# Performance work log

Measured on AMD Instinct MI355X. Metric: run time of the kernel, lower is better.

Reference implementation:

```python
import jax, jax.numpy as jnp
import numpy as np
from functools import partial

IMG_H, IMG_W = 800.0, 800.0
PRE_NMS_TOP_N = 6000
POST_NMS_TOP_N = 1000
MIN_BOX_SIZE = 16.0
NMS_THRESH = 0.7
B, N = 4, 100000


def setup_inputs() -> dict:
    key = jax.random.key(0)
    k1, k2, k3 = jax.random.split(key, 3)
    # plausible boxes: centers in image, sizes in [1, 201] so some fail the min-size test
    ctr = jax.random.uniform(k1, (B, N, 2), dtype=jnp.float32) * jnp.array([IMG_W, IMG_H], jnp.float32)
    wh = jax.random.uniform(k2, (B, N, 2), dtype=jnp.float32) * 200.0 + 1.0
    batch_proposals = jnp.concatenate([ctr - wh / 2.0, ctr + wh / 2.0], axis=-1)  # [B,N,4] x1,y1,x2,y2
    batch_cls_prob = jax.random.uniform(k3, (B, N, 2), dtype=jnp.float32)  # [B,N,2] bg/fg
    return {"batch_proposals": batch_proposals, "batch_cls_prob": batch_cls_prob}


def _clip_boxes(boxes):
    # matches torch clamp of x coords to [0,W], y coords to [0,H]
    x = jnp.clip(boxes[:, 0::2], 0.0, IMG_W)  # [N,2] -> x1,x2
    y = jnp.clip(boxes[:, 1::2], 0.0, IMG_H)  # [N,2] -> y1,y2
    return jnp.stack([x, y], axis=2).reshape(boxes.shape)  # interleave back to x1,y1,x2,y2


def _iou_matrix(b):
    x1, y1, x2, y2 = b[:, 0], b[:, 1], b[:, 2], b[:, 3]
    area = jnp.maximum(x2 - x1, 0.0) * jnp.maximum(y2 - y1, 0.0)  # [P]
    xx1 = jnp.maximum(x1[:, None], x1[None, :])
    yy1 = jnp.maximum(y1[:, None], y1[None, :])
    xx2 = jnp.minimum(x2[:, None], x2[None, :])
    yy2 = jnp.minimum(y2[:, None], y2[None, :])
    inter = jnp.maximum(xx2 - xx1, 0.0) * jnp.maximum(yy2 - yy1, 0.0)  # [P,P]
    union = area[:, None] + area[None, :] - inter
    return inter / jnp.maximum(union, 1e-9)


def _greedy_nms_keep(iou, valid):
    # boxes are already sorted by score (descending); standard greedy suppression
    P = iou.shape[0]
    idx = jnp.arange(P)

    def body(i, keep):
        sup = keep[i] & (iou[i] > NMS_THRESH) & (idx > i)
        return keep & ~sup

    return jax.lax.fori_loop(0, P, body, valid)


def _per_image(boxes, scores):
    boxes = _clip_boxes(boxes)  # [N,4]
    w = boxes[:, 2] - boxes[:, 0]
    h = boxes[:, 3] - boxes[:, 1]
    valid = (w >= MIN_BOX_SIZE) & (h >= MIN_BOX_SIZE)
    # filter-then-topk == mask invalid to -inf then topk (assuming >= PRE valid boxes)
    s_masked = jnp.where(valid, scores, -jnp.inf)
    top_s, top_idx = jax.lax.top_k(s_masked, PRE_NMS_TOP_N)
    b = boxes[top_idx]            # [P,4]
    v = valid[top_idx]            # [P]
    keep = _greedy_nms_keep(_iou_matrix(b), v)
    s2 = jnp.where(keep, top_s, -jnp.inf)
    fin_s, fin_idx = jax.lax.top_k(s2, POST_NMS_TOP_N)  # kept boxes, score order
    fin_keep = keep[fin_idx]
    fin_b = jnp.where(fin_keep[:, None], b[fin_idx], 0.0)
    fin_s = jnp.where(fin_keep, fin_s, 0.0)  # zero-pad if fewer than POST kept
    return fin_s, fin_b


def reference(batch_proposals, batch_cls_prob):
    scores = batch_cls_prob[:, :, 1]  # fg prob
    final_scores, final_boxes = jax.vmap(_per_image)(batch_proposals, scores)
    return final_scores, final_boxes  # [B,POST], [B,POST,4]
```

## Files before the change

kernel.cpp:

```cpp
#include <hip/hip_runtime.h>
#include <hip/hip_bf16.h>
#include <math.h>

typedef unsigned int uint;
typedef unsigned short ushort;
typedef unsigned long long u64;

#define BB 4
#define NN 100000
#define PRE 6000
#define POST 1000
#define NWRD 94
#define PREF 2048
#define PWRD 32
#define SCAP 8192
#define ROWP 6016
#define KSUP 64
#define NRANGE 32
#define WQ 16

constexpr size_t OFF_HDR   = 0;
constexpr size_t OFF_RTOT  = 64;
constexpr size_t OFF_CNT   = 1024;
constexpr size_t OFF_H1    = OFF_CNT + (size_t)BB*ROWP*4;
constexpr size_t OFF_BASE  = OFF_H1  + (size_t)BB*65536*4;
constexpr size_t OFF_KEY   = OFF_BASE+ (size_t)BB*65536*4;
constexpr size_t OFF_BKT   = OFF_KEY + (size_t)BB*NN*4;
constexpr size_t OFF_BUCK  = OFF_BKT + (size_t)BB*NN*2;
constexpr size_t OFF_BBOX  = OFF_BUCK+ (size_t)BB*SCAP*8;
constexpr size_t OFF_BSC   = OFF_BBOX+ (size_t)BB*SCAP*16;
constexpr size_t OFF_BBKT  = OFF_BSC + (size_t)BB*SCAP*4;
constexpr size_t OFF_LIST  = OFF_BBKT+ (size_t)BB*SCAP*2;
constexpr size_t OFF_BOX   = OFF_LIST+ (size_t)BB*ROWP*KSUP*4;
constexpr size_t OFF_SCO   = OFF_BOX + (size_t)BB*ROWP*16;
constexpr size_t OFF_AREA  = OFF_SCO + (size_t)BB*ROWP*4;
constexpr size_t OFF_VAL   = OFF_AREA+ (size_t)BB*ROWP*4;

__device__ __forceinline__ float clipf(float v, float hi) {
  return fminf(fmaxf(v, 0.0f), hi);
}

__device__ __forceinline__ uint bucket_of(float s, bool valid) {
  if (!valid) return 65535u;
  float t = fminf(fmaxf(s, 0.0f), 1.0f);
  uint q = (uint)(t * 65536.0f);
  q = q > 65535u ? 65535u : q;
  return 65535u - q;
}

__global__ void keys_only(const float4* __restrict__ props,
                          const float2* __restrict__ clsp,
                          uint* __restrict__ keyhi,
                          ushort* __restrict__ bkts) {
  int b = blockIdx.y;
  int i = blockIdx.x * 256 + threadIdx.x;
  if (i >= NN) return;
  float4 p = props[(size_t)b * NN + i];
  float x1 = clipf(p.x, 800.0f), y1 = clipf(p.y, 800.0f);
  float x2 = clipf(p.z, 800.0f), y2 = clipf(p.w, 800.0f);
  bool valid = ((x2 - x1) >= 16.0f) && ((y2 - y1) >= 16.0f);
  float s  = clsp[(size_t)b * NN + i].y;
  float sm = valid ? s : -INFINITY;
  uint u = __float_as_uint(sm);
  u = (u & 0x80000000u) ? ~u : (u | 0x80000000u);
  keyhi[(size_t)b * NN + i] = ~u;
  bkts[(size_t)b * NN + i] = (ushort)bucket_of(s, valid);
}

__global__ __launch_bounds__(256) void hist_range(const uint4* __restrict__ bkts4,
                                                  uint* __restrict__ hist1,
                                                  uint* __restrict__ rtot,
                                                  uint* __restrict__ cnt) {
  int b = blockIdx.y;
  int r = blockIdx.x;
  uint lo = (uint)r << 11;
  __shared__ uint lh[2048];
  __shared__ uint wr[4];
  int tid = threadIdx.x, lane = tid & 63, W = tid >> 6;
  for (int i = tid; i < 2048; i += 256) lh[i] = 0u;
  __syncthreads();
  const uint4* K = bkts4 + (size_t)b * (NN / 8);
  uint inv = 0;
  for (int i = tid; i < NN / 8; i += 256) {
    uint4 v = K[i];
    uint q;
    q = v.x & 0xFFFFu;  { uint d = q - lo; if (d < 2048u) { if (q == 0xFFFFu) inv++; else atomicAdd(&lh[d], 1u); } }
    q = v.x >> 16;      { uint d = q - lo; if (d < 2048u) { if (q == 0xFFFFu) inv++; else atomicAdd(&lh[d], 1u); } }
    q = v.y & 0xFFFFu;  { uint d = q - lo; if (d < 2048u) { if (q == 0xFFFFu) inv++; else atomicAdd(&lh[d], 1u); } }
    q = v.y >> 16;      { uint d = q - lo; if (d < 2048u) { if (q == 0xFFFFu) inv++; else atomicAdd(&lh[d], 1u); } }
    q = v.z & 0xFFFFu;  { uint d = q - lo; if (d < 2048u) { if (q == 0xFFFFu) inv++; else atomicAdd(&lh[d], 1u); } }
    q = v.z >> 16;      { uint d = q - lo; if (d < 2048u) { if (q == 0xFFFFu) inv++; else atomicAdd(&lh[d], 1u); } }
    q = v.w & 0xFFFFu;  { uint d = q - lo; if (d < 2048u) { if (q == 0xFFFFu) inv++; else atomicAdd(&lh[d], 1u); } }
    q = v.w >> 16;      { uint d = q - lo; if (d < 2048u) { if (q == 0xFFFFu) inv++; else atomicAdd(&lh[d], 1u); } }
  }
  if (inv) atomicAdd(&lh[2047], inv);
  __syncthreads();
  uint* H = hist1 + (size_t)b * 65536 + lo;
  uint s = 0;
  for (int i = tid; i < 2048; i += 256) { H[i] = lh[i]; s += lh[i]; }
  for (int off = 32; off > 0; off >>= 1) s += __shfl_xor(s, off);
  if (lane == 0) wr[W] = s;
  __syncthreads();
  if (tid == 0) rtot[b * 32 + r] = wr[0] + wr[1] + wr[2] + wr[3];
  uint* C = cnt + (size_t)b * ROWP + r * (ROWP / NRANGE);
  if (tid < ROWP / NRANGE) C[tid] = 0u;
}

__global__ __launch_bounds__(256) void scan128(const uint* __restrict__ hist1,
                                               const uint* __restrict__ rtot,
                                               uint* __restrict__ base,
                                               uint* __restrict__ hdr,
                                               u64* __restrict__ validW) {
  int r = blockIdx.x, b = blockIdx.y;
  int tid = threadIdx.x, lane = tid & 63, W = tid >> 6;
  __shared__ uint wt[4];
  if (r == 0 && tid < 96) validW[(size_t)b * 96 + tid] = 0ull;
  uint lo = (uint)r << 11;
  uint rbase = 0, tot = 0;
  for (int k = 0; k < 32; ++k) {
    uint v = rtot[b * 32 + k];
    if (k < r) rbase += v;
    if (k == r) tot = v;
  }
  const uint* h = hist1 + (size_t)b * 65536 + lo;
  uint c[8], s = 0;
  for (int k = 0; k < 8; ++k) { c[k] = h[tid * 8 + k]; s += c[k]; }
  uint ps = s;
  for (int off = 1; off < 64; off <<= 1) {
    uint v = __shfl_up(ps, off);
    if (lane >= off) ps += v;
  }
  if (lane == 63) wt[W] = ps;
  __syncthreads();
  uint wbase = 0;
  for (int k = 0; k < 4; ++k) { if (k < W) wbase += wt[k]; }
  uint excl = rbase + wbase + ps - s;
  uint run = excl;
  uint* bs = base + (size_t)b * 65536 + lo;
  for (int k = 0; k < 8; ++k) { bs[tid * 8 + k] = run; run += c[k]; }
  if (rbase < (uint)PRE && (uint)PRE <= rbase + tot) {
    uint cc = excl;
    for (int k = 0; k < 8; ++k) {
      uint hv = c[k];
      if (cc < (uint)PRE && (uint)PRE <= cc + hv) {
        hdr[0 + b] = lo + (uint)(tid * 8 + k);
        hdr[4 + b] = cc + hv;
      }
      cc += hv;
    }
  }
}

__global__ void bucket_scatter(const uint* __restrict__ keyhi,
                               const ushort* __restrict__ bkts,
                               uint* __restrict__ base,
                               const uint* __restrict__ hdr,
                               const float4* __restrict__ props,
                               const float2* __restrict__ clsp,
                               u64* __restrict__ buck,
                               float4* __restrict__ buckBox,
                               float* __restrict__ buckSc,
                               ushort* __restrict__ buckBkt) {
  int b = blockIdx.y;
  int i = blockIdx.x * 256 + threadIdx.x;
  if (i >= NN) return;
  uint bk = bkts[(size_t)b * NN + i];
  if (bk <= hdr[0 + b]) {
    uint kh = keyhi[(size_t)b * NN + i];
    uint pos = atomicAdd(&base[(size_t)b * 65536 + bk], 1u);
    if (pos < SCAP) {
      buck[(size_t)b * SCAP + pos] = ((u64)kh << 32) | (uint)i;
      float4 p = props[(size_t)b * NN + i];
      float4 bx;
      bx.x = clipf(p.x, 800.0f); bx.y = clipf(p.y, 800.0f);
      bx.z = clipf(p.z, 800.0f); bx.w = clipf(p.w, 800.0f);
      buckBox[(size_t)b * SCAP + pos] = bx;
      buckSc [(size_t)b * SCAP + pos] = clsp[(size_t)b * NN + i].y;
      buckBkt[(size_t)b * SCAP + pos] = (ushort)bk;
    }
  }
}

__global__ void rank_scatter(const u64* __restrict__ buck,
                             const float4* __restrict__ buckBox,
                             const float* __restrict__ buckSc,
                             const ushort* __restrict__ buckBkt,
                             const uint* __restrict__ base,
                             const uint* __restrict__ hist,
                             const uint* __restrict__ hdr,
                             float4* __restrict__ boxes6k,
                             float* __restrict__ score6k,
                             float* __restrict__ area6k,
                             u64* __restrict__ validW) {
  int b = blockIdx.y;
  int s = blockIdx.x * 256 + threadIdx.x;
  uint limit = hdr[4 + b];
  if (s >= (int)limit) return;
  u64 v = buck[(size_t)b * SCAP + s];
  float4 bx = buckBox[(size_t)b * SCAP + s];
  float sc = buckSc[(size_t)b * SCAP + s];
  uint bkt = buckBkt[(size_t)b * SCAP + s];
  uint cntb = hist[(size_t)b * 65536 + bkt];
  uint b0 = base[(size_t)b * 65536 + bkt] - cntb;
  uint r = b0;
  for (uint m = 0; m < cntb; ++m) {
    u64 w = buck[(size_t)b * SCAP + b0 + m];
    r += (w < v) ? 1u : 0u;
  }
  if (r >= (uint)PRE) return;
  float w = bx.z - bx.x, h = bx.w - bx.y;
  bool valid = (w >= 16.0f) && (h >= 16.0f);
  boxes6k[(size_t)b * ROWP + r] = bx;
  score6k[(size_t)b * ROWP + r] = sc;
  area6k [(size_t)b * ROWP + r] = fmaxf(w, 0.0f) * fmaxf(h, 0.0f);
  if (valid) atomicOr(&validW[(size_t)b * 96 + (r >> 6)], 1ull << (r & 63));
}

__device__ __forceinline__
void sup_tile(int b, int gb, int cw0, int wmax,
              const float4* boxes6k, const float* area6k, const u64* validW,
              uint* cnt, uint* list,
              float4* rbox, float* rar ) {
  int w = threadIdx.x >> 6, lane = threadIdx.x & 63;
  if (threadIdx.x < 64) {
    rbox[lane] = boxes6k[(size_t)b * ROWP + gb * 64 + lane];
    rar[lane]  = area6k [(size_t)b * ROWP + gb * 64 + lane];
  }
  __syncthreads();
  u64 vmask = validW[(size_t)b * 96 + gb];

  int    cw[4];
  u64    rowsel[4], bits[4];
  float4 cbox[4];
  float  carea[4];
  #pragma unroll
  for (int k = 0; k < 4; ++k) {
    cw[k] = cw0 + 4 * k + w;
    int col = cw[k] * 64 + lane;
    int colc = col < (ROWP - 1) ? col : (ROWP - 1);
    cbox[k]  = boxes6k[(size_t)b * ROWP + colc];
    carea[k] = area6k [(size_t)b * ROWP + colc];
    rowsel[k] = (cw[k] > gb) ? vmask
              : ((cw[k] == gb && lane) ? (vmask & ((1ull << lane) - 1ull)) : 0ull);
    bits[k] = 0ull;
  }

  const double M = 0x1.6666668p-1;
  #pragma unroll 4
  for (int r = 0; r < 64; ++r) {
    float4 rb = rbox[r];
    float  ra = rar[r];
    u64 m = 1ull << r;
    #pragma unroll
    for (int k = 0; k < 4; ++k) {
      float xx1 = fmaxf(rb.x, cbox[k].x), yy1 = fmaxf(rb.y, cbox[k].y);
      float xx2 = fminf(rb.z, cbox[k].z), yy2 = fminf(rb.w, cbox[k].w);
      float inter = fmaxf(xx2 - xx1, 0.0f) * fmaxf(yy2 - yy1, 0.0f);
      float un = fmaxf(ra + carea[k] - inter, 1e-9f);
      bits[k] |= ((double)inter >= M * (double)un) ? m : 0ull;
    }
  }

  int rbase = gb * 64;
  #pragma unroll
  for (int k = 0; k < 4; ++k) {
    if (cw[k] >= wmax) continue;
    u64 bt = bits[k] & rowsel[k];
    int col = cw[k] * 64 + lane;
    while (bt) {
      int r = __ffsll((long long)bt) - 1;
      bt &= bt - 1;
      uint pos = atomicAdd(&cnt[(size_t)b * ROWP + col], 1u);
      if (pos < KSUP) list[((size_t)b * ROWP + col) * KSUP + pos] = (uint)(rbase + r);
    }
  }
}

__global__ __launch_bounds__(256) void sup_build_pre(const float4* __restrict__ boxes6k,
                                                     const float* __restrict__ area6k,
                                                     const u64* __restrict__ validW,
                                                     uint* __restrict__ cnt,
                                                     uint* __restrict__ list) {
  int gb = blockIdx.y, b = blockIdx.z;
  int cw0 = blockIdx.x * WQ;
  if (cw0 + WQ - 1 < gb) return;
  __shared__ float4 rbox[64];
  __shared__ float  rar[64];
  sup_tile(b, gb, cw0, PWRD, boxes6k, area6k, validW, cnt, list, rbox, rar);
}

__global__ __launch_bounds__(256) void sup_build_full(const float4* __restrict__ boxes6k,
                                                      const float* __restrict__ area6k,
                                                      const u64* __restrict__ validW,
                                                      const uint* __restrict__ hdr,
                                                      uint* __restrict__ cnt,
                                                      uint* __restrict__ list) {
  int gb = blockIdx.y, b = blockIdx.z;
  if (hdr[8 + b]) return;
  int cw0 = blockIdx.x * WQ;
  if (cw0 + WQ - 1 < gb) return;
  if (gb < PWRD && cw0 + WQ <= PWRD) return;
  __shared__ float4 rbox[64];
  __shared__ float  rar[64];
  sup_tile(b, gb, cw0, NWRD, boxes6k, area6k, validW, cnt, list, rbox, rar);
}

__global__ __launch_bounds__(1024) void resolve_pre(const uint* __restrict__ cnt,
                                                    const uint* __restrict__ list,
                                                    const u64* __restrict__ validW,
                                                    const float* __restrict__ score6k,
                                                    const float4* __restrict__ boxes6k,
                                                    uint* __restrict__ hdr,
                                                    float* __restrict__ out) {
  int b = blockIdx.x, tid = threadIdx.x;
  __shared__ u64 ALIVE[PWRD], DEC[PWRD], VW[PWRD];
  __shared__ int changed;
  if (tid < PWRD) {
    ALIVE[tid] = 0ull; DEC[tid] = 0ull;
    VW[tid] = validW[(size_t)b * 96 + tid];
  }
  __syncthreads();

  uint myCnt[2];
  #pragma unroll
  for (int r = 0; r < 2; ++r) {
    int j = tid + r * 1024;
    myCnt[r] = (j < PREF) ? cnt[(size_t)b * ROWP + j] : 0u;
  }
  #pragma unroll
  for (int r = 0; r < 2; ++r) {
    int j = tid + r * 1024;
    if (j >= PREF) continue;
    bool valid = (VW[j >> 6] >> (j & 63)) & 1ull;
    if (myCnt[r] == 0u || !valid) {
      atomicOr(&DEC[j >> 6], 1ull << (j & 63));
      if (valid) atomicOr(&ALIVE[j >> 6], 1ull << (j & 63));
    }
  }
  __syncthreads();

  while (true) {
    if (tid == 0) changed = 0;
    __syncthreads();
    int decJ[2]; bool decAlive[2];
    #pragma unroll
    for (int r = 0; r < 2; ++r) {
      decJ[r] = -1; decAlive[r] = false;
      int j = tid + r * 1024;
      if (j >= PREF || myCnt[r] == 0u) continue;
      if ((DEC[j >> 6] >> (j & 63)) & 1ull) continue;
      const uint* lj = list + ((size_t)b * ROWP + j) * KSUP;
      uint c = myCnt[r] < KSUP ? myCnt[r] : KSUP;
      bool anyAlive = false, pending = false;
      for (uint m = 0; m < c; ++m) {
        uint i = lj[m];
        bool ai = (ALIVE[i >> 6] >> (i & 63)) & 1ull;
        bool di = (DEC[i >> 6] >> (i & 63)) & 1ull;
        if (ai) { anyAlive = true; break; }
        if (!di) pending = true;
      }
      if (anyAlive)      { decJ[r] = j; decAlive[r] = false; }
      else if (!pending) { decJ[r] = j; decAlive[r] = true;  }
    }
    __syncthreads();
    bool any = false;
    #pragma unroll
    for (int r = 0; r < 2; ++r) {
      if (decJ[r] >= 0) {
        int j = decJ[r];
        if (decAlive[r]) atomicOr(&ALIVE[j >> 6], 1ull << (j & 63));
        atomicOr(&DEC[j >> 6], 1ull << (j & 63));
        any = true;
      }
    }
    if (any) atomicAdd(&changed, 1);
    __syncthreads();
    if (changed == 0) break;
  }

  __shared__ uint psum[PWRD + 1];
  if (tid == 0) {
    uint c = 0;
    for (int w = 0; w < PWRD; ++w) { psum[w] = c; c += (uint)__popcll(ALIVE[w]); }
    psum[PWRD] = c;
    hdr[8 + b] = (c >= (uint)POST) ? 1u : 0u;
  }
  __syncthreads();
  if (psum[PWRD] < (uint)POST) return;

  for (int q = tid; q < POST; q += 1024) out[(size_t)b * POST + q] = 0.0f;
  for (int t = tid; t < POST * 4; t += 1024) out[(size_t)BB * POST + (size_t)b * POST * 4 + t] = 0.0f;
  __syncthreads();
  for (int j = tid; j < PREF; j += 1024) {
    int w = j >> 6, bit = j & 63;
    u64 word = ALIVE[w];
    if ((word >> bit) & 1ull) {
      uint rank = psum[w] + (uint)__popcll(word & ((1ull << bit) - 1ull));
      if (rank < POST) {
        out[(size_t)b * POST + rank] = score6k[(size_t)b * ROWP + j];
        float4 bx = boxes6k[(size_t)b * ROWP + j];
        float* o = out + (size_t)BB * POST + ((size_t)b * POST + rank) * 4;
        o[0] = bx.x; o[1] = bx.y; o[2] = bx.z; o[3] = bx.w;
      }
    }
  }
}

__global__ __launch_bounds__(1024) void resolve_full(const uint* __restrict__ cnt,
                                                     const uint* __restrict__ list,
                                                     const u64* __restrict__ validW,
                                                     const float* __restrict__ score6k,
                                                     const float4* __restrict__ boxes6k,
                                                     const uint* __restrict__ hdr,
                                                     float* __restrict__ out) {
  int b = blockIdx.x, tid = threadIdx.x;
  if (hdr[8 + b]) return;
  __shared__ u64 ALIVE[96], DEC[96], VW[96];
  __shared__ int changed;
  if (tid < 96) {
    ALIVE[tid] = 0ull; DEC[tid] = 0ull;
    VW[tid] = validW[(size_t)b * 96 + tid];
  }
  __syncthreads();

  uint myCnt[6];
  #pragma unroll
  for (int r = 0; r < 6; ++r) {
    int j = tid + r * 1024;
    myCnt[r] = (j < PRE) ? cnt[(size_t)b * ROWP + j] : 0u;
  }
  #pragma unroll
  for (int r = 0; r < 6; ++r) {
    int j = tid + r * 1024;
    if (j >= PRE) continue;
    bool valid = (VW[j >> 6] >> (j & 63)) & 1ull;
    if (myCnt[r] == 0u || !valid) {
      atomicOr(&DEC[j >> 6], 1ull << (j & 63));
      if (valid) atomicOr(&ALIVE[j >> 6], 1ull << (j & 63));
    }
  }
  __syncthreads();

  while (true) {
    if (tid == 0) changed = 0;
    __syncthreads();
    int decJ[6]; bool decAlive[6];
    #pragma unroll
    for (int r = 0; r < 6; ++r) {
      decJ[r] = -1; decAlive[r] = false;
      int j = tid + r * 1024;
      if (j >= PRE || myCnt[r] == 0u) continue;
      if ((DEC[j >> 6] >> (j & 63)) & 1ull) continue;
      const uint* lj = list + ((size_t)b * ROWP + j) * KSUP;
      uint c = myCnt[r] < KSUP ? myCnt[r] : KSUP;
      bool anyAlive = false, pending = false;
      for (uint m = 0; m < c; ++m) {
        uint i = lj[m];
        bool ai = (ALIVE[i >> 6] >> (i & 63)) & 1ull;
        bool di = (DEC[i >> 6] >> (i & 63)) & 1ull;
        if (ai) { anyAlive = true; break; }
        if (!di) pending = true;
      }
      if (anyAlive)      { decJ[r] = j; decAlive[r] = false; }
      else if (!pending) { decJ[r] = j; decAlive[r] = true;  }
    }
    __syncthreads();
    bool any = false;
    #pragma unroll
    for (int r = 0; r < 6; ++r) {
      if (decJ[r] >= 0) {
        int j = decJ[r];
        if (decAlive[r]) atomicOr(&ALIVE[j >> 6], 1ull << (j & 63));
        atomicOr(&DEC[j >> 6], 1ull << (j & 63));
        any = true;
      }
    }
    if (any) atomicAdd(&changed, 1);
    __syncthreads();
    if (changed == 0) break;
  }

  __shared__ uint psum[NWRD + 1];
  if (tid == 0) {
    uint c = 0;
    for (int w = 0; w < NWRD; ++w) { psum[w] = c; c += (uint)__popcll(ALIVE[w]); }
    psum[NWRD] = c;
  }
  __syncthreads();
  for (int q = tid; q < POST; q += 1024) out[(size_t)b * POST + q] = 0.0f;
  for (int t = tid; t < POST * 4; t += 1024) out[(size_t)BB * POST + (size_t)b * POST * 4 + t] = 0.0f;
  __syncthreads();
  for (int j = tid; j < PRE; j += 1024) {
    int w = j >> 6, bit = j & 63;
    u64 word = ALIVE[w];
    if ((word >> bit) & 1ull) {
      uint rank = psum[w] + (uint)__popcll(word & ((1ull << bit) - 1ull));
      if (rank < POST) {
        out[(size_t)b * POST + rank] = score6k[(size_t)b * ROWP + j];
        float4 bx = boxes6k[(size_t)b * ROWP + j];
        float* o = out + (size_t)BB * POST + ((size_t)b * POST + rank) * 4;
        o[0] = bx.x; o[1] = bx.y; o[2] = bx.z; o[3] = bx.w;
      }
    }
  }
}

extern "C" void kernel_launch(void* const* d_in, const int* in_sizes, int n_in,
                              void* d_out, int out_size, void* d_ws, size_t ws_size,
                              hipStream_t stream) {
  const float4* props = (const float4*)d_in[0];
  const float2* clsp  = (const float2*)d_in[1];
  float* out = (float*)d_out;
  char* ws = (char*)d_ws;

  uint*   hdr     = (uint*)(ws + OFF_HDR);
  uint*   rtot    = (uint*)(ws + OFF_RTOT);
  uint*   cnt     = (uint*)(ws + OFF_CNT);
  uint*   hist1   = (uint*)(ws + OFF_H1);
  uint*   base    = (uint*)(ws + OFF_BASE);
  uint*   keyhi   = (uint*)(ws + OFF_KEY);
  ushort* bkts    = (ushort*)(ws + OFF_BKT);
  u64*    buck    = (u64*) (ws + OFF_BUCK);
  float4* buckBox = (float4*)(ws + OFF_BBOX);
  float*  buckSc  = (float*)(ws + OFF_BSC);
  ushort* buckBkt = (ushort*)(ws + OFF_BBKT);
  uint*   list    = (uint*)(ws + OFF_LIST);
  float4* boxes6k = (float4*)(ws + OFF_BOX);
  float*  score6k = (float*)(ws + OFF_SCO);
  float*  area6k  = (float*)(ws + OFF_AREA);
  u64*    validW  = (u64*) (ws + OFF_VAL);

  dim3 gN((NN + 255) / 256, BB);
  keys_only<<<gN, 256, 0, stream>>>(props, clsp, keyhi, bkts);
  hist_range<<<dim3(NRANGE, BB), 256, 0, stream>>>((const uint4*)bkts, hist1, rtot, cnt);
  scan128<<<dim3(NRANGE, BB), 256, 0, stream>>>(hist1, rtot, base, hdr, validW);
  bucket_scatter<<<gN, 256, 0, stream>>>(keyhi, bkts, base, hdr, props, clsp,
                                         buck, buckBox, buckSc, buckBkt);
  rank_scatter<<<dim3(SCAP / 256, BB), 256, 0, stream>>>(buck, buckBox, buckSc, buckBkt,
                                                         base, hist1, hdr,
                                                         boxes6k, score6k, area6k, validW);
  sup_build_pre<<<dim3(2, PWRD, BB), 256, 0, stream>>>(boxes6k, area6k, validW, cnt, list);
  resolve_pre<<<BB, 1024, 0, stream>>>(cnt, list, validW, score6k, boxes6k, hdr, out);
  sup_build_full<<<dim3((NWRD + WQ - 1) / WQ, NWRD, BB), 256, 0, stream>>>(boxes6k, area6k,
                                                                           validW, hdr, cnt, list);
  resolve_full<<<BB, 1024, 0, stream>>>(cnt, list, validW, score6k, boxes6k, hdr, out);
}
```

Before: 95.61 us.

## Fuse fallback suppression build and full resolve into resolve_pre; drop key pass

Stops precomputing the 32-bit sort keys in the first pass and instead computes them only for boxes that reach bucket_scatter, which removes a full-size workspace write and read. The fallback path (used when the first 2048 candidates yield fewer than POST survivors) is moved inside resolve_pre: the same block builds the remaining IoU suppression lists and then runs the full resolve. This removes two kernel launches and the header flag handshake. The cost is that the fallback tile work now runs on only one block per image instead of a wide grid, so it becomes much slower whenever that path is taken.

Result: faster. 92.48 us (-3.3%).

```diff
diff --git a/kernel.cpp b/kernel.cpp
--- a/kernel.cpp
+++ b/kernel.cpp
@@ -24,8 +24,7 @@
 constexpr size_t OFF_CNT   = 1024;
 constexpr size_t OFF_H1    = OFF_CNT + (size_t)BB*ROWP*4;
 constexpr size_t OFF_BASE  = OFF_H1  + (size_t)BB*65536*4;
-constexpr size_t OFF_KEY   = OFF_BASE+ (size_t)BB*65536*4;
-constexpr size_t OFF_BKT   = OFF_KEY + (size_t)BB*NN*4;
+constexpr size_t OFF_BKT   = OFF_BASE+ (size_t)BB*65536*4;
 constexpr size_t OFF_BUCK  = OFF_BKT + (size_t)BB*NN*2;
 constexpr size_t OFF_BBOX  = OFF_BUCK+ (size_t)BB*SCAP*8;
 constexpr size_t OFF_BSC   = OFF_BBOX+ (size_t)BB*SCAP*16;
@@ -48,9 +47,8 @@
   return 65535u - q;
 }
 
-__global__ void keys_only(const float4* __restrict__ props,
+__global__ void bkts_only(const float4* __restrict__ props,
                           const float2* __restrict__ clsp,
-                          uint* __restrict__ keyhi,
                           ushort* __restrict__ bkts) {
   int b = blockIdx.y;
   int i = blockIdx.x * 256 + threadIdx.x;
@@ -60,10 +58,6 @@
   float x2 = clipf(p.z, 800.0f), y2 = clipf(p.w, 800.0f);
   bool valid = ((x2 - x1) >= 16.0f) && ((y2 - y1) >= 16.0f);
   float s  = clsp[(size_t)b * NN + i].y;
-  float sm = valid ? s : -INFINITY;
-  uint u = __float_as_uint(sm);
-  u = (u & 0x80000000u) ? ~u : (u | 0x80000000u);
-  keyhi[(size_t)b * NN + i] = ~u;
   bkts[(size_t)b * NN + i] = (ushort)bucket_of(s, valid);
 }
 
@@ -151,8 +145,7 @@
   }
 }
 
-__global__ void bucket_scatter(const uint* __restrict__ keyhi,
-                               const ushort* __restrict__ bkts,
+__global__ void bucket_scatter(const ushort* __restrict__ bkts,
                                uint* __restrict__ base,
                                const uint* __restrict__ hdr,
                                const float4* __restrict__ props,
@@ -166,16 +159,21 @@
   if (i >= NN) return;
   uint bk = bkts[(size_t)b * NN + i];
   if (bk <= hdr[0 + b]) {
-    uint kh = keyhi[(size_t)b * NN + i];
     uint pos = atomicAdd(&base[(size_t)b * 65536 + bk], 1u);
     if (pos < SCAP) {
-      buck[(size_t)b * SCAP + pos] = ((u64)kh << 32) | (uint)i;
       float4 p = props[(size_t)b * NN + i];
       float4 bx;
       bx.x = clipf(p.x, 800.0f); bx.y = clipf(p.y, 800.0f);
       bx.z = clipf(p.z, 800.0f); bx.w = clipf(p.w, 800.0f);
+      bool valid = ((bx.z - bx.x) >= 16.0f) && ((bx.w - bx.y) >= 16.0f);
+      float s = clsp[(size_t)b * NN + i].y;
+      float sm = valid ? s : -INFINITY;
+      uint u = __float_as_uint(sm);
+      u = (u & 0x80000000u) ? ~u : (u | 0x80000000u);
+      uint kh = ~u;
+      buck[(size_t)b * SCAP + pos] = ((u64)kh << 32) | (uint)i;
       buckBox[(size_t)b * SCAP + pos] = bx;
-      buckSc [(size_t)b * SCAP + pos] = clsp[(size_t)b * NN + i].y;
+      buckSc [(size_t)b * SCAP + pos] = s;
       buckBkt[(size_t)b * SCAP + pos] = (ushort)bk;
     }
   }
@@ -289,33 +287,20 @@
   sup_tile(b, gb, cw0, PWRD, boxes6k, area6k, validW, cnt, list, rbox, rar);
 }
 
-__global__ __launch_bounds__(256) void sup_build_full(const float4* __restrict__ boxes6k,
-                                                      const float* __restrict__ area6k,
-                                                      const u64* __restrict__ validW,
-                                                      const uint* __restrict__ hdr,
-                                                      uint* __restrict__ cnt,
-                                                      uint* __restrict__ list) {
-  int gb = blockIdx.y, b = blockIdx.z;
-  if (hdr[8 + b]) return;
-  int cw0 = blockIdx.x * WQ;
-  if (cw0 + WQ - 1 < gb) return;
-  if (gb < PWRD && cw0 + WQ <= PWRD) return;
-  __shared__ float4 rbox[64];
-  __shared__ float  rar[64];
-  sup_tile(b, gb, cw0, NWRD, boxes6k, area6k, validW, cnt, list, rbox, rar);
-}
-
-__global__ __launch_bounds__(1024) void resolve_pre(const uint* __restrict__ cnt,
-                                                    const uint* __restrict__ list,
+__global__ __launch_bounds__(1024) void resolve_pre(uint* __restrict__ cnt,
+                                                    uint* __restrict__ list,
                                                     const u64* __restrict__ validW,
                                                     const float* __restrict__ score6k,
                                                     const float4* __restrict__ boxes6k,
-                                                    uint* __restrict__ hdr,
+                                                    const float* __restrict__ area6k,
                                                     float* __restrict__ out) {
-  int b = blockIdx.x, tid = threadIdx.x;
-  __shared__ u64 ALIVE[PWRD], DEC[PWRD], VW[PWRD];
+  int b = blockIdx.x, tid = threadIdx.x, lane = tid & 63, wv = tid >> 6;
+  __shared__ u64 ALIVE[96], DEC[96], VW[96];
   __shared__ int changed;
-  if (tid < PWRD) {
+  __shared__ uint psum[NWRD + 1];
+  __shared__ float4 rbox[64];
+  __shared__ float  rar[64];
+  if (tid < 96) {
     ALIVE[tid] = 0ull; DEC[tid] = 0ull;
     VW[tid] = validW[(size_t)b * 96 + tid];
   }
@@ -338,7 +323,6 @@
     }
   }
   __syncthreads();
-
   while (true) {
     if (tid == 0) changed = 0;
     __syncthreads();
@@ -378,69 +362,90 @@
     if (changed == 0) break;
   }
 
-  __shared__ uint psum[PWRD + 1];
   if (tid == 0) {
     uint c = 0;
     for (int w = 0; w < PWRD; ++w) { psum[w] = c; c += (uint)__popcll(ALIVE[w]); }
     psum[PWRD] = c;
-    hdr[8 + b] = (c >= (uint)POST) ? 1u : 0u;
-  }
-  __syncthreads();
-  if (psum[PWRD] < (uint)POST) return;
-
-  for (int q = tid; q < POST; q += 1024) out[(size_t)b * POST + q] = 0.0f;
-  for (int t = tid; t < POST * 4; t += 1024) out[(size_t)BB * POST + (size_t)b * POST * 4 + t] = 0.0f;
-  __syncthreads();
-  for (int j = tid; j < PREF; j += 1024) {
-    int w = j >> 6, bit = j & 63;
-    u64 word = ALIVE[w];
-    if ((word >> bit) & 1ull) {
-      uint rank = psum[w] + (uint)__popcll(word & ((1ull << bit) - 1ull));
-      if (rank < POST) {
-        out[(size_t)b * POST + rank] = score6k[(size_t)b * ROWP + j];
-        float4 bx = boxes6k[(size_t)b * ROWP + j];
-        float* o = out + (size_t)BB * POST + ((size_t)b * POST + rank) * 4;
-        o[0] = bx.x; o[1] = bx.y; o[2] = bx.z; o[3] = bx.w;
-      }
-    }
-  }
-}
-
-__global__ __launch_bounds__(1024) void resolve_full(const uint* __restrict__ cnt,
-                                                     const uint* __restrict__ list,
-                                                     const u64* __restrict__ validW,
-                                                     const float* __restrict__ score6k,
-                                                     const float4* __restrict__ boxes6k,
-                                                     const uint* __restrict__ hdr,
-                                                     float* __restrict__ out) {
-  int b = blockIdx.x, tid = threadIdx.x;
-  if (hdr[8 + b]) return;
-  __shared__ u64 ALIVE[96], DEC[96], VW[96];
-  __shared__ int changed;
-  if (tid < 96) {
-    ALIVE[tid] = 0ull; DEC[tid] = 0ull;
-    VW[tid] = validW[(size_t)b * 96 + tid];
-  }
-  __syncthreads();
-
-  uint myCnt[6];
+  }
+  __syncthreads();
+
+  if (psum[PWRD] >= (uint)POST) {
+    for (int q = tid; q < POST; q += 1024) out[(size_t)b * POST + q] = 0.0f;
+    for (int t = tid; t < POST * 4; t += 1024) out[(size_t)BB * POST + (size_t)b * POST * 4 + t] = 0.0f;
+    __syncthreads();
+    for (int j = tid; j < PREF; j += 1024) {
+      int w = j >> 6, bit = j & 63;
+      u64 word = ALIVE[w];
+      if ((word >> bit) & 1ull) {
+        uint rank = psum[w] + (uint)__popcll(word & ((1ull << bit) - 1ull));
+        if (rank < POST) {
+          out[(size_t)b * POST + rank] = score6k[(size_t)b * ROWP + j];
+          float4 bx = boxes6k[(size_t)b * ROWP + j];
+          float* o = out + (size_t)BB * POST + ((size_t)b * POST + rank) * 4;
+          o[0] = bx.x; o[1] = bx.y; o[2] = bx.z; o[3] = bx.w;
+        }
+      }
+    }
+    return;
+  }
+
+  const double M = 0x1.6666668p-1;
+  for (int gb = 0; gb < NWRD; ++gb) {
+    __syncthreads();
+    if (tid < 64) {
+      rbox[tid] = boxes6k[(size_t)b * ROWP + gb * 64 + tid];
+      rar[tid]  = area6k [(size_t)b * ROWP + gb * 64 + tid];
+    }
+    __syncthreads();
+    u64 vmask = VW[gb];
+    for (int cw = gb + wv; cw < NWRD; cw += 16) {
+      if (gb < PWRD && cw < PWRD) continue;
+      int col = cw * 64 + lane;
+      int colc = col < (ROWP - 1) ? col : (ROWP - 1);
+      float4 c = boxes6k[(size_t)b * ROWP + colc];
+      float ca = area6k[(size_t)b * ROWP + colc];
+      u64 rowsel = (cw > gb) ? vmask
+                 : (lane ? (vmask & ((1ull << lane) - 1ull)) : 0ull);
+      u64 bits = 0;
+      #pragma unroll 4
+      for (int r = 0; r < 64; ++r) {
+        float4 rb = rbox[r];
+        float xx1 = fmaxf(rb.x, c.x), yy1 = fmaxf(rb.y, c.y);
+        float xx2 = fminf(rb.z, c.z), yy2 = fminf(rb.w, c.w);
+        float inter = fmaxf(xx2 - xx1, 0.0f) * fmaxf(yy2 - yy1, 0.0f);
+        float un = fmaxf(rar[r] + ca - inter, 1e-9f);
+        bits |= ((double)inter >= M * (double)un) ? (1ull << r) : 0ull;
+      }
+      bits &= rowsel;
+      while (bits) {
+        int r = __ffsll((long long)bits) - 1;
+        bits &= bits - 1;
+        uint pos = atomicAdd(&cnt[(size_t)b * ROWP + col], 1u);
+        if (pos < KSUP) list[((size_t)b * ROWP + col) * KSUP + pos] = (uint)(gb * 64 + r);
+      }
+    }
+  }
+  __syncthreads();
+
+  if (tid < 96) { ALIVE[tid] = 0ull; DEC[tid] = 0ull; }
+  __syncthreads();
+  uint myCnt6[6];
   #pragma unroll
   for (int r = 0; r < 6; ++r) {
     int j = tid + r * 1024;
-    myCnt[r] = (j < PRE) ? cnt[(size_t)b * ROWP + j] : 0u;
+    myCnt6[r] = (j < PRE) ? cnt[(size_t)b * ROWP + j] : 0u;
   }
   #pragma unroll
   for (int r = 0; r < 6; ++r) {
     int j = tid + r * 1024;
     if (j >= PRE) continue;
     bool valid = (VW[j >> 6] >> (j & 63)) & 1ull;
-    if (myCnt[r] == 0u || !valid) {
+    if (myCnt6[r] == 0u || !valid) {
       atomicOr(&DEC[j >> 6], 1ull << (j & 63));
       if (valid) atomicOr(&ALIVE[j >> 6], 1ull << (j & 63));
     }
   }
   __syncthreads();
-
   while (true) {
     if (tid == 0) changed = 0;
     __syncthreads();
@@ -449,10 +454,10 @@
     for (int r = 0; r < 6; ++r) {
       decJ[r] = -1; decAlive[r] = false;
       int j = tid + r * 1024;
-      if (j >= PRE || myCnt[r] == 0u) continue;
+      if (j >= PRE || myCnt6[r] == 0u) continue;
       if ((DEC[j >> 6] >> (j & 63)) & 1ull) continue;
       const uint* lj = list + ((size_t)b * ROWP + j) * KSUP;
-      uint c = myCnt[r] < KSUP ? myCnt[r] : KSUP;
+      uint c = myCnt6[r] < KSUP ? myCnt6[r] : KSUP;
       bool anyAlive = false, pending = false;
       for (uint m = 0; m < c; ++m) {
         uint i = lj[m];
@@ -480,7 +485,6 @@
     if (changed == 0) break;
   }
 
-  __shared__ uint psum[NWRD + 1];
   if (tid == 0) {
     uint c = 0;
     for (int w = 0; w < NWRD; ++w) { psum[w] = c; c += (uint)__popcll(ALIVE[w]); }
@@ -518,7 +522,6 @@
   uint*   cnt     = (uint*)(ws + OFF_CNT);
   uint*   hist1   = (uint*)(ws + OFF_H1);
   uint*   base    = (uint*)(ws + OFF_BASE);
-  uint*   keyhi   = (uint*)(ws + OFF_KEY);
   ushort* bkts    = (ushort*)(ws + OFF_BKT);
   u64*    buck    = (u64*) (ws + OFF_BUCK);
   float4* buckBox = (float4*)(ws + OFF_BBOX);
@@ -531,17 +534,14 @@
   u64*    validW  = (u64*) (ws + OFF_VAL);
 
   dim3 gN((NN + 255) / 256, BB);
-  keys_only<<<gN, 256, 0, stream>>>(props, clsp, keyhi, bkts);
+  bkts_only<<<gN, 256, 0, stream>>>(props, clsp, bkts);
   hist_range<<<dim3(NRANGE, BB), 256, 0, stream>>>((const uint4*)bkts, hist1, rtot, cnt);
   scan128<<<dim3(NRANGE, BB), 256, 0, stream>>>(hist1, rtot, base, hdr, validW);
-  bucket_scatter<<<gN, 256, 0, stream>>>(keyhi, bkts, base, hdr, props, clsp,
+  bucket_scatter<<<gN, 256, 0, stream>>>(bkts, base, hdr, props, clsp,
                                          buck, buckBox, buckSc, buckBkt);
   rank_scatter<<<dim3(SCAP / 256, BB), 256, 0, stream>>>(buck, buckBox, buckSc, buckBkt,
                                                          base, hist1, hdr,
                                                          boxes6k, score6k, area6k, validW);
   sup_build_pre<<<dim3(2, PWRD, BB), 256, 0, stream>>>(boxes6k, area6k, validW, cnt, list);
-  resolve_pre<<<BB, 1024, 0, stream>>>(cnt, list, validW, score6k, boxes6k, hdr, out);
-  sup_build_full<<<dim3((NWRD + WQ - 1) / WQ, NWRD, BB), 256, 0, stream>>>(boxes6k, area6k,
-                                                                           validW, hdr, cnt, list);
-  resolve_full<<<BB, 1024, 0, stream>>>(cnt, list, validW, score6k, boxes6k, hdr, out);
-}
+  resolve_pre<<<BB, 1024, 0, stream>>>(cnt, list, validW, score6k, boxes6k, area6k, out);
+}
```
